# Performance work log

Hardware: AMD Instinct MI355X
Metric: run time of the kernel (lower is better)

The kernel has to match this reference:

```python
import jax, jax.numpy as jnp
import numpy as np

TEMP = 0.07


def setup_inputs() -> dict:
    key = jax.random.key(0)
    kq, kk = jax.random.split(key)
    B, D = 8192, 128
    q = jax.random.normal(kq, (B, D), dtype=jnp.float32)
    k = jax.random.normal(kk, (B, D), dtype=jnp.float32)
    return {"q": q, "k": k}


def reference(q, k):
    # features = cat([q, k], dim=0); F.normalize(dim=1)
    B = q.shape[0]
    N = 2 * B
    f = jnp.concatenate([q, k], axis=0)
    f = f / jnp.maximum(jnp.linalg.norm(f, axis=1, keepdims=True), 1e-12)
    sim = f @ f.T  # [N, N]

    i = jnp.arange(N)
    p = (i + B) % N                      # index of the positive pair of row i
    pos = sim[i, p][:, None]             # [N, 1]

    # negatives: all columns except the diagonal (i) and the positive (p),
    # in original column order (matches boolean-mask ordering in torch).
    a = jnp.minimum(i, p)[:, None]       # [N, 1]
    b = jnp.maximum(i, p)[:, None]
    j = jnp.arange(N - 2)[None, :]       # [1, N-2]
    c = j + (j >= a)                     # skip first excluded column
    c = c + (c >= b)                     # skip second excluded column
    neg = jnp.take_along_axis(sim, c, axis=1)  # [N, N-2]

    logits = jnp.concatenate([pos, neg], axis=1) / TEMP  # [N, N-1]
    labels = jnp.zeros((N,), dtype=jnp.int32)
    return logits, labels
```

## Files before the change

### kernel.cpp

```cpp
#include <hip/hip_runtime.h>
#include <hip/hip_bf16.h>
#include <stdint.h>

#define B_ROWS 8192
#define N_TOT  16384
#define D_DIM  128
#define INV_TEMP (1.0f / 0.07f)

typedef __bf16 bf16x8 __attribute__((ext_vector_type(8)));
typedef float  f32x4  __attribute__((ext_vector_type(4)));

__global__ void simclr_norm_kernel(const float* __restrict__ q,
                                   const float* __restrict__ k,
                                   unsigned int* __restrict__ fb) {
    const int lane = threadIdx.x & 63;
    const int row  = blockIdx.x * 4 + (threadIdx.x >> 6);
    const float* src = (row < B_ROWS) ? (q + (size_t)row * D_DIM)
                                      : (k + (size_t)(row - B_ROWS) * D_DIM);
    float2 v = ((const float2*)src)[lane];
    float s = v.x * v.x + v.y * v.y;
#pragma unroll
    for (int off = 32; off > 0; off >>= 1) s += __shfl_xor(s, off);
    float rn = 1.0f / fmaxf(sqrtf(s), 1e-12f);
    union { __bf16 h[2]; unsigned int u; } pk;
    pk.h[0] = (__bf16)(v.x * rn);
    pk.h[1] = (__bf16)(v.y * rn);
    fb[(size_t)row * 64 + lane] = pk.u;
}

__global__ __launch_bounds__(256, 2) void simclr_gemm_kernel(
        const unsigned short* __restrict__ fb, float* __restrict__ out) {
    __shared__ char lds[65536];

    const int brow = blockIdx.x >> 7;
    const int bcol = blockIdx.x & 127;
    const int tid  = threadIdx.x;
    const int lane = tid & 63;
    const int w    = tid >> 6;

    {
        const int chunk = lane & 15;
        const int rsub  = lane >> 4;
#pragma unroll
        for (int i = 0; i < 8; ++i) {
            const int r = w * 32 + i * 4 + rsub;
            const int src_chunk = chunk ^ (r & 7);
            const char* gA = (const char*)(fb + ((size_t)(brow * 128 + r) * D_DIM + src_chunk * 8));
            const char* gB = (const char*)(fb + ((size_t)(bcol * 128 + r) * D_DIM + src_chunk * 8));
            char* lA = lds + (w * 32 + i * 4) * 256;
            char* lB = lds + 32768 + (w * 32 + i * 4) * 256;
            __builtin_amdgcn_global_load_lds((const __attribute__((address_space(1))) void*)gA,
                                             (__attribute__((address_space(3))) void*)lA, 16, 0, 0);
            __builtin_amdgcn_global_load_lds((const __attribute__((address_space(1))) void*)gB,
                                             (__attribute__((address_space(3))) void*)lB, 16, 0, 0);
        }
    }
    __syncthreads();

    const int wr = w >> 1, wc = w & 1;
    const int rl = lane & 15;
    const int kg = lane >> 4;

    f32x4 acc[4][4];
#pragma unroll
    for (int m = 0; m < 4; ++m)
#pragma unroll
        for (int n = 0; n < 4; ++n) acc[m][n] = (f32x4){0.f, 0.f, 0.f, 0.f};

#pragma unroll
    for (int ks = 0; ks < 4; ++ks) {
        bf16x8 afr[4], bfr[4];
        const int kb = ks * 64 + kg * 16;
#pragma unroll
        for (int m = 0; m < 4; ++m) {
            const int r = wr * 64 + m * 16 + rl;
            afr[m] = *(const bf16x8*)(lds + r * 256 + (kb ^ ((r & 7) << 4)));
        }
#pragma unroll
        for (int n = 0; n < 4; ++n) {
            const int r = wc * 64 + n * 16 + rl;
            bfr[n] = *(const bf16x8*)(lds + 32768 + r * 256 + (kb ^ ((r & 7) << 4)));
        }
#pragma unroll
        for (int m = 0; m < 4; ++m)
#pragma unroll
            for (int n = 0; n < 4; ++n)
                acc[m][n] = __builtin_amdgcn_mfma_f32_16x16x32_bf16(afr[m], bfr[n], acc[m][n], 0, 0, 0);
    }

    const int i0 = brow * 128 + wr * 64 + (kg << 2);
    const int c0 = bcol * 128 + wc * 64 + rl;
#pragma unroll
    for (int m = 0; m < 4; ++m) {
#pragma unroll
        for (int r = 0; r < 4; ++r) {
            const int i = i0 + m * 16 + r;
            const int p = i ^ B_ROWS;
            const int a = i & (B_ROWS - 1);
            const int b = a | B_ROWS;
            float* orow = out + (size_t)i * (N_TOT - 1);
#pragma unroll
            for (int n = 0; n < 4; ++n) {
                const int c = c0 + n * 16;
                const float v = acc[m][n][r] * INV_TEMP;
                if (c == i) continue;
                const int col = (c == p) ? 0 : (c + 1 - (c > a) - (c > b));
                orow[col] = v;
            }
        }
    }
}

__global__ void simclr_zero_labels(float* __restrict__ out) {
    out[(size_t)N_TOT * (N_TOT - 1) + blockIdx.x * 256 + threadIdx.x] = 0.0f;
}

extern "C" void kernel_launch(void* const* d_in, const int* in_sizes, int n_in,
                              void* d_out, int out_size, void* d_ws, size_t ws_size,
                              hipStream_t stream) {
    const float* q = (const float*)d_in[0];
    const float* k = (const float*)d_in[1];
    float* out = (float*)d_out;
    unsigned int* fb = (unsigned int*)d_ws;

    simclr_norm_kernel<<<N_TOT / 4, 256, 0, stream>>>(q, k, fb);
    simclr_zero_labels<<<N_TOT / 256, 256, 0, stream>>>(out);
    simclr_gemm_kernel<<<128 * 128, 256, 0, stream>>>((const unsigned short*)d_ws, out);
}
```

Before: 357.4 us.

## Transpose MFMA output so each lane stores four contiguous columns; fold temperature into normalization

The MFMA operands are swapped so each lane's accumulator holds four consecutive columns of one row instead of four rows of one column. The epilogue can then write 16-byte chunks per lane, with a rare slow path for chunks containing the diagonal or positive column. The 1/temperature scale is folded into the normalization as sqrt(1/T), which removes the per-element multiply but changes bf16 rounding slightly. Output rows have stride N-1 and column shifts, so the vector stores are generally misaligned to 16 bytes.

After: 366.0 us. 1.02x slower.

```diff
diff --git a/kernel.cpp b/kernel.cpp
--- a/kernel.cpp
+++ b/kernel.cpp
@@ -5,7 +5,7 @@
 #define B_ROWS 8192
 #define N_TOT  16384
 #define D_DIM  128
-#define INV_TEMP (1.0f / 0.07f)
+#define SCALE_SQRT_INVT 3.7796447300922722f
 
 typedef __bf16 bf16x8 __attribute__((ext_vector_type(8)));
 typedef float  f32x4  __attribute__((ext_vector_type(4)));
@@ -21,7 +21,7 @@
     float s = v.x * v.x + v.y * v.y;
 #pragma unroll
     for (int off = 32; off > 0; off >>= 1) s += __shfl_xor(s, off);
-    float rn = 1.0f / fmaxf(sqrtf(s), 1e-12f);
+    float rn = SCALE_SQRT_INVT / fmaxf(sqrtf(s), 1e-12f);
     union { __bf16 h[2]; unsigned int u; } pk;
     pk.h[0] = (__bf16)(v.x * rn);
     pk.h[1] = (__bf16)(v.y * rn);
@@ -85,27 +85,34 @@
         for (int m = 0; m < 4; ++m)
 #pragma unroll
             for (int n = 0; n < 4; ++n)
-                acc[m][n] = __builtin_amdgcn_mfma_f32_16x16x32_bf16(afr[m], bfr[n], acc[m][n], 0, 0, 0);
+                acc[m][n] = __builtin_amdgcn_mfma_f32_16x16x32_bf16(bfr[n], afr[m], acc[m][n], 0, 0, 0);
     }
 
-    const int i0 = brow * 128 + wr * 64 + (kg << 2);
-    const int c0 = bcol * 128 + wc * 64 + rl;
+    const int i_base = brow * 128 + wr * 64 + rl;
+    const int c_base = bcol * 128 + wc * 64 + (kg << 2);
 #pragma unroll
     for (int m = 0; m < 4; ++m) {
+        const int i = i_base + m * 16;
+        const int p = i ^ B_ROWS;
+        const int a = i & (B_ROWS - 1);
+        const int b = a | B_ROWS;
+        float* orow = out + (size_t)i * (N_TOT - 1);
 #pragma unroll
-        for (int r = 0; r < 4; ++r) {
-            const int i = i0 + m * 16 + r;
-            const int p = i ^ B_ROWS;
-            const int a = i & (B_ROWS - 1);
-            const int b = a | B_ROWS;
-            float* orow = out + (size_t)i * (N_TOT - 1);
+        for (int n = 0; n < 4; ++n) {
+            const int c = c_base + n * 16;
+            f32x4 v = acc[m][n];
+            if (__builtin_expect((unsigned)(a - c) < 4u || (unsigned)(b - c) < 4u, 0)) {
 #pragma unroll
-            for (int n = 0; n < 4; ++n) {
-                const int c = c0 + n * 16;
-                const float v = acc[m][n][r] * INV_TEMP;
-                if (c == i) continue;
-                const int col = (c == p) ? 0 : (c + 1 - (c > a) - (c > b));
-                orow[col] = v;
+                for (int e = 0; e < 4; ++e) {
+                    const int cc = c + e;
+                    const float val = v[e];
+                    if (cc == i) continue;
+                    if (cc == p) { orow[0] = val; continue; }
+                    orow[cc + 1 - (cc > a) - (cc > b)] = val;
+                }
+            } else {
+                const int s = 1 - (c > a) - (c > b);
+                __builtin_memcpy(orow + c + s, &v, sizeof(v));
             }
         }
     }
```
